# Optimization experiments

Hardware: AMD Instinct MI355X
Metric: run time of the kernel (lower is better)

Reference implementation:

```python
import jax, jax.numpy as jnp
import numpy as np

H = 8          # n_heads
D = 1024       # dim_tgt == dim_mem
DQ = D // H    # per-head dim = 128
BN = 512       # LFFN bottleneck (hardcoded in module)
HID = 1024     # LFFN hidden (hardcoded in module)
B = 16
S_T = 1024     # target length
S_M = 2048     # memory length
SCALE = DQ ** 0.25  # module uses dim_q ** (1/4)
EPS = 1e-5


def _ln(x, g, b):
    m = jnp.mean(x, axis=-1, keepdims=True)
    v = jnp.mean(jnp.square(x - m), axis=-1, keepdims=True)
    return (x - m) * jax.lax.rsqrt(v + EPS) * g + b


def _mhla(xq, xk, xv, Wq, Wk, Wv, Wo, masked):
    # per-head projections: x [b,s,D] x W [H,D,DQ] -> [b,H,s,DQ]
    Q = jnp.einsum('bsq,hqd->bhsd', xq, Wq)
    K = jnp.einsum('bsq,hqd->bhsd', xk, Wk)
    V = jnp.einsum('bsq,hqd->bhsd', xv, Wv)
    if masked:
        s, d = Q.shape[-2], Q.shape[-1]
        # module adds log(triu(ones).T) directly to Q: 0 where d_idx<=t, -inf otherwise
        m = jnp.where(jnp.arange(d)[None, :] <= jnp.arange(s)[:, None], 0.0, -jnp.inf)
        Q = Q + m.astype(Q.dtype)
    # softmax_col(K^T/d_k) over head-dim axis == softmax(K/d_k, axis=-1)
    A = jnp.einsum('bhsd,bhse->bhde', jax.nn.softmax(K / SCALE, axis=-1), V)  # [b,H,DQ,DQ]
    Bm = jnp.einsum('bhsd,bhde->bhse', jax.nn.softmax(Q / SCALE, axis=-1), A)  # [b,H,s,DQ]
    b, h, w, dd = Bm.shape
    # torch .view(b, w, h*d) on contiguous [b,h,w,d]: raw row-major reshape (no transpose)
    Bm = Bm.reshape(b, w, h * dd)
    return Bm @ Wo.T


def setup_inputs():
    key = jax.random.key(0)
    ks = jax.random.split(key, 24)
    r = lambda k, sh, s=0.02: (jax.random.normal(k, sh, jnp.float32) * s)
    return {
        'mem': jax.random.normal(ks[0], (B, S_M, D), jnp.float32),
        'y': jax.random.normal(ks[1], (B, S_T, D), jnp.float32),
        # self-attention (masked)
        'Wq1': r(ks[2], (H, D, DQ)), 'Wk1': r(ks[3], (H, D, DQ)), 'Wv1': r(ks[4], (H, D, DQ)),
        'Wo1': r(ks[5], (D, D)),
        # cross-attention with memory
        'Wq2': r(ks[6], (H, D, DQ)), 'Wk2': r(ks[7], (H, D, DQ)), 'Wv2': r(ks[8], (H, D, DQ)),
        'Wo2': r(ks[9], (D, D)),
        # LFFN (torch Linear weights are [out, in])
        'E1': r(ks[10], (BN, D)), 'D1': r(ks[11], (HID, BN)),
        'E2': r(ks[12], (BN, HID)), 'D2': r(ks[13], (D, BN)),
        # LayerNorm affine params
        'g1': jnp.ones((D,), jnp.float32), 'b1': jnp.zeros((D,), jnp.float32),
        'g2': jnp.ones((D,), jnp.float32), 'b2': jnp.zeros((D,), jnp.float32),
        'g3': jnp.ones((D,), jnp.float32), 'b3': jnp.zeros((D,), jnp.float32),
    }


def reference(mem, y, Wq1, Wk1, Wv1, Wo1, Wq2, Wk2, Wv2, Wo2,
              E1, D1, E2, D2, g1, b1, g2, b2, g3, b3):
    # dropout layers are identity in eval mode
    y = y + _mhla(y, y, y, Wq1, Wk1, Wv1, Wo1, masked=True)
    y = _ln(y, g1, b1)
    y = y + _mhla(y, mem, mem, Wq2, Wk2, Wv2, Wo2, masked=False)
    y = _ln(y, g2, b2)
    # LFFN: E1 -> D1 -> swish -> E2 -> D2
    h = (y @ E1.T) @ D1.T
    h = h * jax.nn.sigmoid(h)
    ffn = (h @ E2.T) @ D2.T
    y = _ln(y + ffn, g3, b3)
    return y
```

## Files before the change

### kernel.cpp

```cpp
#include <hip/hip_runtime.h>
#include <hip/hip_bf16.h>

#define DEVI __device__ __forceinline__

typedef __bf16 bfrag __attribute__((ext_vector_type(8)));
typedef unsigned short us8 __attribute__((ext_vector_type(8)));
typedef float f32x4 __attribute__((ext_vector_type(4)));
typedef unsigned short ushort_t;

static constexpr int NB  = 16;
static constexpr int NH  = 8;
static constexpr int DIM = 1024;
static constexpr int DQh = 128;
static constexpr int ST  = 1024;
static constexpr int SM  = 2048;
static constexpr float INV_SCALE = 0.29730177875068026f;
static constexpr float LN_EPS = 1e-5f;

DEVI ushort_t f2bf(float f) {
  __hip_bfloat16 h = __float2bfloat16(f);
  return __builtin_bit_cast(ushort_t, h);
}
DEVI float bf2f(ushort_t u) {
  return __bfloat162float(__builtin_bit_cast(__hip_bfloat16, u));
}
DEVI bfrag ldfrag(const ushort_t* p) {
  return __builtin_bit_cast(bfrag, *(const us8*)p);
}
DEVI void gl16(const ushort_t* g, ushort_t* l) {
  __builtin_amdgcn_global_load_lds(
      (const __attribute__((address_space(1))) void*)g,
      (__attribute__((address_space(3))) void*)l, 16, 0, 0);
}

enum { ST_BF16 = 0, ST_SWISH = 1, ST_F32RES = 2, ST_SCR = 3, ST_QKV = 4 };

template<int STORE>
__global__ __launch_bounds__(256, 2)
void gemm_bb(const ushort_t* __restrict__ A, const ushort_t* __restrict__ Bt,
             const float* __restrict__ Res,
             ushort_t* __restrict__ Q0, ushort_t* __restrict__ Q1,
             ushort_t* __restrict__ Q2, float* __restrict__ Cf,
             int M, int N, int K, long aZ, long bZ, int logS)
{
  __shared__ ushort_t As[128][32];
  __shared__ ushort_t Bs[128][32];
  const int tid = threadIdx.x;
  int bx = blockIdx.x, by = blockIdx.y;
  if (gridDim.z == 1) {
    const int gx = gridDim.x;
    const int nwg = gx * gridDim.y;
    int bid = by * gx + bx;
    if ((nwg & 7) == 0) bid = (bid & 7) * (nwg >> 3) + (bid >> 3);
    bx = bid % gx; by = bid / gx;
  }
  const int z = blockIdx.z;
  const int m0 = by * 128, n0 = bx * 128;
  A  += aZ * (long)z;
  Bt += bZ * (long)z;

  const int lane = tid & 63;
  const int w = tid >> 6;
  const int wr = (w >> 1) * 64, wc = (w & 1) * 64;
  const int frow = lane & 15;

  const int grow = lane >> 2;
  const int gk = ((lane & 3) ^ ((lane >> 3) & 3)) * 8;
  const ushort_t* Ag = A + (long)(m0 + w * 32 + grow) * K + gk;
  const ushort_t* Bg = Bt + (long)(n0 + w * 32 + grow) * K + gk;

  f32x4 acc[4][4];
  #pragma unroll
  for (int i = 0; i < 4; ++i)
    #pragma unroll
    for (int j = 0; j < 4; ++j) acc[i][j] = f32x4{0.f, 0.f, 0.f, 0.f};

  const int kqs = ((frow >> 1) & 3);
  for (int k0 = 0; k0 < K; k0 += 32) {
    __syncthreads();
    gl16(Ag + k0,               &As[w * 32][0]);
    gl16(Ag + k0 + (long)16 * K, &As[w * 32 + 16][0]);
    gl16(Bg + k0,               &Bs[w * 32][0]);
    gl16(Bg + k0 + (long)16 * K, &Bs[w * 32 + 16][0]);
    __syncthreads();
    const int kq = (lane >> 4) ^ kqs;
    bfrag af[4], bf[4];
    #pragma unroll
    for (int i = 0; i < 4; ++i) af[i] = ldfrag(&As[wr + i * 16 + frow][kq * 8]);
    #pragma unroll
    for (int j = 0; j < 4; ++j) bf[j] = ldfrag(&Bs[wc + j * 16 + frow][kq * 8]);
    #pragma unroll
    for (int i = 0; i < 4; ++i)
      #pragma unroll
      for (int j = 0; j < 4; ++j)
        acc[i][j] = __builtin_amdgcn_mfma_f32_16x16x32_bf16(af[i], bf[j], acc[i][j], 0, 0, 0);
  }

  const int rb = (lane >> 4) * 4;
  if constexpr (STORE == ST_QKV) {
    const int sel = n0 >> 10;
    const int h = (n0 >> 7) & 7;
    ushort_t* __restrict__ Bq = (sel == 0) ? Q0 : ((sel == 1) ? Q1 : Q2);
    const int S = 1 << logS;
    #pragma unroll
    for (int i = 0; i < 4; ++i)
      #pragma unroll
      for (int j = 0; j < 4; ++j)
        #pragma unroll
        for (int e = 0; e < 4; ++e) {
          const int gm = m0 + wr + i * 16 + rb + e;
          const int dq = wc + j * 16 + frow;
          const int b = gm >> logS, s = gm & (S - 1);
          Bq[((long)(h * 16 + b) * S + (long)s) * 128 + dq] = f2bf(acc[i][j][e]);
        }
  } else {
    #pragma unroll
    for (int i = 0; i < 4; ++i)
      #pragma unroll
      for (int j = 0; j < 4; ++j)
        #pragma unroll
        for (int e = 0; e < 4; ++e) {
          const int gm = m0 + wr + i * 16 + rb + e;
          const int gn = n0 + wc + j * 16 + frow;
          float val = acc[i][j][e];
          if constexpr (STORE == ST_SWISH) val = val / (1.0f + __expf(-val));
          if constexpr (STORE == ST_BF16 || STORE == ST_SWISH) {
            Q0[(long)gm * N + gn] = f2bf(val);
          } else if constexpr (STORE == ST_F32RES) {
            Cf[(long)gm * N + gn] = val + Res[(long)gm * N + gn];
          } else if constexpr (STORE == ST_SCR) {
            const int b = z & 15, hh = z >> 4;
            Q0[(long)b * (ST * DIM) + (long)(hh * 128 + (gm >> 3)) * DIM +
               (gm & 7) * 128 + gn] = f2bf(val);
          }
        }
  }
}

__global__ __launch_bounds__(256, 2)
void gemm_ktv(const ushort_t* __restrict__ Kp, const ushort_t* __restrict__ Vp,
              ushort_t* __restrict__ AT, int S)
{
  __shared__ ushort_t As[128][40];
  __shared__ ushort_t Bs[128][40];
  const int tid = threadIdx.x;
  const int z = blockIdx.x;
  const ushort_t* Vb = Vp + (long)z * S * DQh;
  const ushort_t* Kb = Kp + (long)z * S * DQh;
  const int lane = tid & 63;
  const int wr = ((tid >> 6) >> 1) * 64, wc = ((tid >> 6) & 1) * 64;
  const int frow = lane & 15, fk = (lane >> 4) * 8;
  const int c = tid & 127;
  const int sr0 = tid >> 7;

  f32x4 acc[4][4];
  #pragma unroll
  for (int i = 0; i < 4; ++i)
    #pragma unroll
    for (int j = 0; j < 4; ++j) acc[i][j] = f32x4{0.f, 0.f, 0.f, 0.f};

  for (int s0 = 0; s0 < S; s0 += 32) {
    __syncthreads();
    #pragma unroll
    for (int p = 0; p < 16; ++p) {
      const int sr = sr0 + p * 2;
      As[c][sr] = Vb[(long)(s0 + sr) * DQh + c];
      Bs[c][sr] = Kb[(long)(s0 + sr) * DQh + c];
    }
    __syncthreads();
    bfrag af[4], bfv[4];
    #pragma unroll
    for (int i = 0; i < 4; ++i) af[i]  = ldfrag(&As[wr + i * 16 + frow][fk]);
    #pragma unroll
    for (int j = 0; j < 4; ++j) bfv[j] = ldfrag(&Bs[wc + j * 16 + frow][fk]);
    #pragma unroll
    for (int i = 0; i < 4; ++i)
      #pragma unroll
      for (int j = 0; j < 4; ++j)
        acc[i][j] = __builtin_amdgcn_mfma_f32_16x16x32_bf16(af[i], bfv[j], acc[i][j], 0, 0, 0);
  }
  const int rb = (lane >> 4) * 4;
  #pragma unroll
  for (int i = 0; i < 4; ++i)
    #pragma unroll
    for (int j = 0; j < 4; ++j)
      #pragma unroll
      for (int e = 0; e < 4; ++e)
        AT[(long)z * 16384 + (long)(wr + i * 16 + rb + e) * 128 + (wc + j * 16 + frow)] =
            f2bf(acc[i][j][e]);
}

template<bool MASKED>
__global__ __launch_bounds__(256)
void softmax128(ushort_t* __restrict__ X, int smask)
{
  const int row = blockIdx.x * 4 + (threadIdx.x >> 6);
  const int lane = threadIdx.x & 63;
  ushort_t* xr = X + (long)row * 128;
  float x0 = bf2f(xr[lane]) * INV_SCALE;
  float x1 = bf2f(xr[lane + 64]) * INV_SCALE;
  if constexpr (MASKED) {
    const int s = row & smask;
    if (lane > s)      x0 = -3.0e38f;
    if (lane + 64 > s) x1 = -3.0e38f;
  }
  float mx = fmaxf(x0, x1);
  #pragma unroll
  for (int o = 32; o; o >>= 1) mx = fmaxf(mx, __shfl_xor(mx, o));
  const float e0 = __expf(x0 - mx);
  const float e1 = __expf(x1 - mx);
  float sm = e0 + e1;
  #pragma unroll
  for (int o = 32; o; o >>= 1) sm += __shfl_xor(sm, o);
  const float inv = 1.0f / sm;
  xr[lane]      = f2bf(e0 * inv);
  xr[lane + 64] = f2bf(e1 * inv);
}

__global__ __launch_bounds__(256)
void layernorm_k(const float* __restrict__ X, const float* __restrict__ G,
                 const float* __restrict__ Bta, float* __restrict__ Y,
                 ushort_t* __restrict__ Yb)
{
  const int row = blockIdx.x;
  const int t = threadIdx.x;
  const float4 v = *(const float4*)(X + (long)row * DIM + t * 4);
  float s  = v.x + v.y + v.z + v.w;
  float sq = v.x * v.x + v.y * v.y + v.z * v.z + v.w * v.w;
  #pragma unroll
  for (int o = 32; o; o >>= 1) { s += __shfl_xor(s, o); sq += __shfl_xor(sq, o); }
  __shared__ float ps[4], pq[4];
  if ((t & 63) == 0) { ps[t >> 6] = s; pq[t >> 6] = sq; }
  __syncthreads();
  s  = ps[0] + ps[1] + ps[2] + ps[3];
  sq = pq[0] + pq[1] + pq[2] + pq[3];
  const float mean = s * (1.0f / DIM);
  const float var  = sq * (1.0f / DIM) - mean * mean;
  const float rstd = rsqrtf(var + LN_EPS);
  const float4 gv = *(const float4*)(G + t * 4);
  const float4 bv = *(const float4*)(Bta + t * 4);
  float4 o;
  o.x = (v.x - mean) * rstd * gv.x + bv.x;
  o.y = (v.y - mean) * rstd * gv.y + bv.y;
  o.z = (v.z - mean) * rstd * gv.z + bv.z;
  o.w = (v.w - mean) * rstd * gv.w + bv.w;
  *(float4*)(Y + (long)row * DIM + t * 4) = o;
  if (Yb) {
    ushort4 ob = make_ushort4(f2bf(o.x), f2bf(o.y), f2bf(o.z), f2bf(o.w));
    *(ushort4*)(Yb + (long)row * DIM + t * 4) = ob;
  }
}

__global__ __launch_bounds__(256)
void transpose_cast(const float* __restrict__ W, ushort_t* __restrict__ Wt)
{
  __shared__ float tile[32][33];
  const int z = blockIdx.z;
  const int kb = blockIdx.y * 32;
  const int nb = blockIdx.x * 32;
  const float* src = W + (long)z * DIM * DQh;
  ushort_t* dst = Wt + (long)z * DIM * DQh;
  const int tx = threadIdx.x & 31;
  const int ty = threadIdx.x >> 5;
  #pragma unroll
  for (int r = 0; r < 32; r += 8)
    tile[ty + r][tx] = src[(long)(kb + ty + r) * DQh + nb + tx];
  __syncthreads();
  #pragma unroll
  for (int r = 0; r < 32; r += 8)
    dst[(long)(nb + ty + r) * DIM + kb + tx] = f2bf(tile[tx][ty + r]);
}

__global__ __launch_bounds__(256)
void cast_bf16(const float* __restrict__ X, ushort_t* __restrict__ Yq)
{
  const long i = ((long)blockIdx.x * 256 + threadIdx.x) * 4;
  const float4 v = *(const float4*)(X + i);
  ushort4 sv = make_ushort4(f2bf(v.x), f2bf(v.y), f2bf(v.z), f2bf(v.w));
  *(ushort4*)(Yq + i) = sv;
}


extern "C" void kernel_launch(void* const* d_in, const int* in_sizes, int n_in,
                              void* d_out, int out_size, void* d_ws, size_t ws_size,
                              hipStream_t stream)
{
  (void)in_sizes; (void)n_in; (void)out_size; (void)ws_size;
  const float* mem = (const float*)d_in[0];
  const float* y0  = (const float*)d_in[1];
  const float* Wq1 = (const float*)d_in[2];
  const float* Wk1 = (const float*)d_in[3];
  const float* Wv1 = (const float*)d_in[4];
  const float* Wo1 = (const float*)d_in[5];
  const float* Wq2 = (const float*)d_in[6];
  const float* Wk2 = (const float*)d_in[7];
  const float* Wv2 = (const float*)d_in[8];
  const float* Wo2 = (const float*)d_in[9];
  const float* E1  = (const float*)d_in[10];
  const float* D1  = (const float*)d_in[11];
  const float* E2  = (const float*)d_in[12];
  const float* D2  = (const float*)d_in[13];
  const float* g1  = (const float*)d_in[14];
  const float* b1  = (const float*)d_in[15];
  const float* g2  = (const float*)d_in[16];
  const float* b2  = (const float*)d_in[17];
  const float* g3  = (const float*)d_in[18];
  const float* b3  = (const float*)d_in[19];

  char* ws = (char*)d_ws;
  const size_t MB = 1ull << 20;
  ushort_t* wcat1 = (ushort_t*)(ws + 0 * MB);
  ushort_t* wkv2  = (ushort_t*)(ws + 6 * MB);
  ushort_t* wq2t  = (ushort_t*)(ws + 10 * MB);
  ushort_t* wo1b  = (ushort_t*)(ws + 12 * MB);
  ushort_t* wo2b  = (ushort_t*)(ws + 14 * MB);
  ushort_t* e1b   = (ushort_t*)(ws + 16 * MB);
  ushort_t* d1b   = (ushort_t*)(ws + 17 * MB);
  ushort_t* e2b   = (ushort_t*)(ws + 18 * MB);
  ushort_t* d2b   = (ushort_t*)(ws + 19 * MB);
  ushort_t* y0b   = (ushort_t*)(ws + 20 * MB);
  ushort_t* memb  = (ushort_t*)(ws + 52 * MB);
  ushort_t* qbuf  = (ushort_t*)(ws + 116 * MB);
  ushort_t* kbuf  = (ushort_t*)(ws + 148 * MB);
  ushort_t* vbuf  = (ushort_t*)(ws + 212 * MB);
  ushort_t* amatT = (ushort_t*)(ws + 276 * MB);
  ushort_t* attnb = (ushort_t*)(ws + 280 * MB);
  float*    ybuf  = (float*)(ws + 312 * MB);
  ushort_t* ybf   = (ushort_t*)(ws + 376 * MB);
  ushort_t* hbuf  = (ushort_t*)(ws + 408 * MB);
  ushort_t* bn1   = attnb;
  ushort_t* bn2   = qbuf;

  cast_bf16<<<16384, 256, 0, stream>>>(y0, y0b);
  cast_bf16<<<32768, 256, 0, stream>>>(mem, memb);
  transpose_cast<<<dim3(4, 32, 8), 256, 0, stream>>>(Wq1, wcat1);
  transpose_cast<<<dim3(4, 32, 8), 256, 0, stream>>>(Wk1, wcat1 + (1 << 20));
  transpose_cast<<<dim3(4, 32, 8), 256, 0, stream>>>(Wv1, wcat1 + (2 << 20));
  transpose_cast<<<dim3(4, 32, 8), 256, 0, stream>>>(Wk2, wkv2);
  transpose_cast<<<dim3(4, 32, 8), 256, 0, stream>>>(Wv2, wkv2 + (1 << 20));
  transpose_cast<<<dim3(4, 32, 8), 256, 0, stream>>>(Wq2, wq2t);
  cast_bf16<<<1024, 256, 0, stream>>>(Wo1, wo1b);
  cast_bf16<<<1024, 256, 0, stream>>>(Wo2, wo2b);
  cast_bf16<<<512, 256, 0, stream>>>(E1, e1b);
  cast_bf16<<<512, 256, 0, stream>>>(D1, d1b);
  cast_bf16<<<512, 256, 0, stream>>>(E2, e2b);
  cast_bf16<<<512, 256, 0, stream>>>(D2, d2b);

  gemm_bb<ST_QKV><<<dim3(24, 128, 1), 256, 0, stream>>>(
      y0b, wcat1, nullptr, qbuf, kbuf, vbuf, nullptr,
      NB * ST, 3072, DIM, 0, 0, 10);
  softmax128<true><<<NH * NB * ST / 4, 256, 0, stream>>>(qbuf, ST - 1);
  softmax128<false><<<NH * NB * ST / 4, 256, 0, stream>>>(kbuf, 0);
  gemm_ktv<<<NH * NB, 256, 0, stream>>>(kbuf, vbuf, amatT, ST);
  gemm_bb<ST_SCR><<<dim3(1, 8, 128), 256, 0, stream>>>(
      qbuf, amatT, nullptr, attnb, nullptr, nullptr, nullptr,
      ST, DQh, DQh, (long)ST * DQh, 16384, 0);
  gemm_bb<ST_F32RES><<<dim3(8, 128, 1), 256, 0, stream>>>(
      attnb, wo1b, y0, nullptr, nullptr, nullptr, ybuf,
      NB * ST, DIM, DIM, 0, 0, 0);
  layernorm_k<<<NB * ST, 256, 0, stream>>>(ybuf, g1, b1, ybuf, ybf);

  gemm_bb<ST_QKV><<<dim3(8, 128, 1), 256, 0, stream>>>(
      ybf, wq2t, nullptr, qbuf, nullptr, nullptr, nullptr,
      NB * ST, 1024, DIM, 0, 0, 10);
  gemm_bb<ST_QKV><<<dim3(16, 256, 1), 256, 0, stream>>>(
      memb, wkv2, nullptr, kbuf, vbuf, nullptr, nullptr,
      NB * SM, 2048, DIM, 0, 0, 11);
  softmax128<false><<<NH * NB * ST / 4, 256, 0, stream>>>(qbuf, 0);
  softmax128<false><<<NH * NB * SM / 4, 256, 0, stream>>>(kbuf, 0);
  gemm_ktv<<<NH * NB, 256, 0, stream>>>(kbuf, vbuf, amatT, SM);
  gemm_bb<ST_SCR><<<dim3(1, 8, 128), 256, 0, stream>>>(
      qbuf, amatT, nullptr, attnb, nullptr, nullptr, nullptr,
      ST, DQh, DQh, (long)ST * DQh, 16384, 0);
  gemm_bb<ST_F32RES><<<dim3(8, 128, 1), 256, 0, stream>>>(
      attnb, wo2b, ybuf, nullptr, nullptr, nullptr, ybuf,
      NB * ST, DIM, DIM, 0, 0, 0);
  layernorm_k<<<NB * ST, 256, 0, stream>>>(ybuf, g2, b2, ybuf, ybf);

  gemm_bb<ST_BF16><<<dim3(4, 128, 1), 256, 0, stream>>>(
      ybf, e1b, nullptr, bn1, nullptr, nullptr, nullptr,
      NB * ST, 512, DIM, 0, 0, 0);
  gemm_bb<ST_SWISH><<<dim3(8, 128, 1), 256, 0, stream>>>(
      bn1, d1b, nullptr, hbuf, nullptr, nullptr, nullptr,
      NB * ST, DIM, 512, 0, 0, 0);
  gemm_bb<ST_BF16><<<dim3(4, 128, 1), 256, 0, stream>>>(
      hbuf, e2b, nullptr, bn2, nullptr, nullptr, nullptr,
      NB * ST, 512, DIM, 0, 0, 0);
  gemm_bb<ST_F32RES><<<dim3(8, 128, 1), 256, 0, stream>>>(
      bn2, d2b, ybuf, nullptr, nullptr, nullptr, ybuf,
      NB * ST, DIM, 512, 0, 0, 0);
  layernorm_k<<<NB * ST, 256, 0, stream>>>(ybuf, g3, b3, (float*)d_out, nullptr);
}
```

Baseline: 1.007 ms.

## Fuse head softmax into QKV GEMM epilogue, split K^T V, use bf16 residual stream

The per-row softmax over the head dimension for Q and K now runs inside the QKV projection GEMM epilogue. Row max and sum are combined across the two column warps through shared memory, which removes the separate softmax kernels and their extra read and write of Q and K. The K^T·V reduction is split along sequence chunks into fp32 partials plus a small reduce kernel, giving more blocks to fill the GPU. The residual and LayerNorm path now keeps activations in bf16 instead of fp32 to cut memory traffic, at the cost of lower precision in the residual sums.

```diff
diff --git a/kernel.cpp b/kernel.cpp
--- a/kernel.cpp
+++ b/kernel.cpp
@@ -33,18 +33,20 @@
       (__attribute__((address_space(3))) void*)l, 16, 0, 0);
 }
 
-enum { ST_BF16 = 0, ST_SWISH = 1, ST_F32RES = 2, ST_SCR = 3, ST_QKV = 4 };
+enum { ST_BF16 = 0, ST_SWISH = 1, ST_RESB = 2, ST_SCR = 3, ST_QKV = 4 };
 
 template<int STORE>
 __global__ __launch_bounds__(256, 2)
 void gemm_bb(const ushort_t* __restrict__ A, const ushort_t* __restrict__ Bt,
-             const float* __restrict__ Res,
-             ushort_t* __restrict__ Q0, ushort_t* __restrict__ Q1,
-             ushort_t* __restrict__ Q2, float* __restrict__ Cf,
-             int M, int N, int K, long aZ, long bZ, int logS)
+             const ushort_t* __restrict__ ResB,
+             ushort_t* __restrict__ P0, ushort_t* __restrict__ P1,
+             ushort_t* __restrict__ P2,
+             int M, int N, int K, long aZ, long bZ,
+             int logS, int smflags, int maskflags)
 {
   __shared__ ushort_t As[128][32];
   __shared__ ushort_t Bs[128][32];
+  __shared__ float msx[4][64][2];
   const int tid = threadIdx.x;
   int bx = blockIdx.x, by = blockIdx.y;
   if (gridDim.z == 1) {
@@ -63,6 +65,7 @@
   const int w = tid >> 6;
   const int wr = (w >> 1) * 64, wc = (w & 1) * 64;
   const int frow = lane & 15;
+  const int q = lane >> 4;
 
   const int grow = lane >> 2;
   const int gk = ((lane & 3) ^ ((lane >> 3) & 3)) * 8;
@@ -78,12 +81,12 @@
   const int kqs = ((frow >> 1) & 3);
   for (int k0 = 0; k0 < K; k0 += 32) {
     __syncthreads();
-    gl16(Ag + k0,               &As[w * 32][0]);
+    gl16(Ag + k0,                &As[w * 32][0]);
     gl16(Ag + k0 + (long)16 * K, &As[w * 32 + 16][0]);
-    gl16(Bg + k0,               &Bs[w * 32][0]);
+    gl16(Bg + k0,                &Bs[w * 32][0]);
     gl16(Bg + k0 + (long)16 * K, &Bs[w * 32 + 16][0]);
     __syncthreads();
-    const int kq = (lane >> 4) ^ kqs;
+    const int kq = (q ^ kqs);
     bfrag af[4], bf[4];
     #pragma unroll
     for (int i = 0; i < 4; ++i) af[i] = ldfrag(&As[wr + i * 16 + frow][kq * 8]);
@@ -96,11 +99,89 @@
         acc[i][j] = __builtin_amdgcn_mfma_f32_16x16x32_bf16(af[i], bf[j], acc[i][j], 0, 0, 0);
   }
 
-  const int rb = (lane >> 4) * 4;
+  const int rb = q * 4;
   if constexpr (STORE == ST_QKV) {
     const int sel = n0 >> 10;
+    const bool dosm   = (smflags >> sel) & 1;
+    const bool domask = (maskflags >> sel) & 1;
+    const int smask = (1 << logS) - 1;
+    if (dosm) {
+      #pragma unroll
+      for (int i = 0; i < 4; ++i)
+        #pragma unroll
+        for (int e = 0; e < 4; ++e) {
+          const int slim = (m0 + wr + i * 16 + rb + e) & smask;
+          #pragma unroll
+          for (int j = 0; j < 4; ++j) {
+            const int dq = wc + j * 16 + frow;
+            float v = acc[i][j][e] * INV_SCALE;
+            if (domask && dq > slim) v = -3.0e38f;
+            acc[i][j][e] = v;
+          }
+        }
+      float m_ie[4][4], s_ie[4][4];
+      #pragma unroll
+      for (int i = 0; i < 4; ++i)
+        #pragma unroll
+        for (int e = 0; e < 4; ++e) {
+          float m = fmaxf(fmaxf(acc[i][0][e], acc[i][1][e]),
+                          fmaxf(acc[i][2][e], acc[i][3][e]));
+          m = fmaxf(m, __shfl_xor(m, 1));
+          m = fmaxf(m, __shfl_xor(m, 2));
+          m = fmaxf(m, __shfl_xor(m, 4));
+          m = fmaxf(m, __shfl_xor(m, 8));
+          m_ie[i][e] = m;
+        }
+      #pragma unroll
+      for (int i = 0; i < 4; ++i)
+        #pragma unroll
+        for (int j = 0; j < 4; ++j)
+          #pragma unroll
+          for (int e = 0; e < 4; ++e)
+            acc[i][j][e] = __expf(acc[i][j][e] - m_ie[i][e]);
+      #pragma unroll
+      for (int i = 0; i < 4; ++i)
+        #pragma unroll
+        for (int e = 0; e < 4; ++e) {
+          float s = acc[i][0][e] + acc[i][1][e] + acc[i][2][e] + acc[i][3][e];
+          s += __shfl_xor(s, 1);
+          s += __shfl_xor(s, 2);
+          s += __shfl_xor(s, 4);
+          s += __shfl_xor(s, 8);
+          s_ie[i][e] = s;
+        }
+      if (frow == 0) {
+        #pragma unroll
+        for (int i = 0; i < 4; ++i)
+          #pragma unroll
+          for (int e = 0; e < 4; ++e) {
+            msx[w][i * 16 + rb + e][0] = m_ie[i][e];
+            msx[w][i * 16 + rb + e][1] = s_ie[i][e];
+          }
+      }
+      __syncthreads();
+      #pragma unroll
+      for (int i = 0; i < 4; ++i)
+        #pragma unroll
+        for (int e = 0; e < 4; ++e) {
+          const int idx = i * 16 + rb + e;
+          const float mo = msx[w ^ 1][idx][0];
+          const float so = msx[w ^ 1][idx][1];
+          const float mj = fmaxf(m_ie[i][e], mo);
+          const float sj = s_ie[i][e] * __expf(m_ie[i][e] - mj) +
+                           so * __expf(mo - mj);
+          m_ie[i][e] = __expf(m_ie[i][e] - mj) / sj;
+        }
+      #pragma unroll
+      for (int i = 0; i < 4; ++i)
+        #pragma unroll
+        for (int j = 0; j < 4; ++j)
+          #pragma unroll
+          for (int e = 0; e < 4; ++e)
+            acc[i][j][e] *= m_ie[i][e];
+    }
     const int h = (n0 >> 7) & 7;
-    ushort_t* __restrict__ Bq = (sel == 0) ? Q0 : ((sel == 1) ? Q1 : Q2);
+    ushort_t* __restrict__ Bq = (sel == 0) ? P0 : ((sel == 1) ? P1 : P2);
     const int S = 1 << logS;
     #pragma unroll
     for (int i = 0; i < 4; ++i)
@@ -115,38 +196,41 @@
         }
   } else {
     #pragma unroll
-    for (int i = 0; i < 4; ++i)
-      #pragma unroll
-      for (int j = 0; j < 4; ++j)
+    for (int i = 0; i < 4; ++i) {
+      #pragma unroll
+      for (int j = 0; j < 4; ++j) {
         #pragma unroll
         for (int e = 0; e < 4; ++e) {
           const int gm = m0 + wr + i * 16 + rb + e;
           const int gn = n0 + wc + j * 16 + frow;
           float val = acc[i][j][e];
           if constexpr (STORE == ST_SWISH) val = val / (1.0f + __expf(-val));
-          if constexpr (STORE == ST_BF16 || STORE == ST_SWISH) {
-            Q0[(long)gm * N + gn] = f2bf(val);
-          } else if constexpr (STORE == ST_F32RES) {
-            Cf[(long)gm * N + gn] = val + Res[(long)gm * N + gn];
-          } else if constexpr (STORE == ST_SCR) {
+          if constexpr (STORE == ST_RESB)  val += bf2f(ResB[(long)gm * N + gn]);
+          if constexpr (STORE == ST_SCR) {
             const int b = z & 15, hh = z >> 4;
-            Q0[(long)b * (ST * DIM) + (long)(hh * 128 + (gm >> 3)) * DIM +
+            P0[(long)b * (ST * DIM) + (long)(hh * 128 + (gm >> 3)) * DIM +
                (gm & 7) * 128 + gn] = f2bf(val);
+          } else {
+            P0[(long)gm * N + gn] = f2bf(val);
           }
         }
+      }
+    }
   }
 }
 
 __global__ __launch_bounds__(256, 2)
 void gemm_ktv(const ushort_t* __restrict__ Kp, const ushort_t* __restrict__ Vp,
-              ushort_t* __restrict__ AT, int S)
+              float* __restrict__ P, int S, int SC)
 {
   __shared__ ushort_t As[128][40];
   __shared__ ushort_t Bs[128][40];
   const int tid = threadIdx.x;
   const int z = blockIdx.x;
-  const ushort_t* Vb = Vp + (long)z * S * DQh;
-  const ushort_t* Kb = Kp + (long)z * S * DQh;
+  const int ch = blockIdx.y;
+  const long base = ((long)z * S + (long)ch * SC) * DQh;
+  const ushort_t* Vb = Vp + base;
+  const ushort_t* Kb = Kp + base;
   const int lane = tid & 63;
   const int wr = ((tid >> 6) >> 1) * 64, wc = ((tid >> 6) & 1) * 64;
   const int frow = lane & 15, fk = (lane >> 4) * 8;
@@ -159,7 +243,7 @@
     #pragma unroll
     for (int j = 0; j < 4; ++j) acc[i][j] = f32x4{0.f, 0.f, 0.f, 0.f};
 
-  for (int s0 = 0; s0 < S; s0 += 32) {
+  for (int s0 = 0; s0 < SC; s0 += 32) {
     __syncthreads();
     #pragma unroll
     for (int p = 0; p < 16; ++p) {
@@ -179,6 +263,7 @@
       for (int j = 0; j < 4; ++j)
         acc[i][j] = __builtin_amdgcn_mfma_f32_16x16x32_bf16(af[i], bfv[j], acc[i][j], 0, 0, 0);
   }
+  float* Pz = P + ((long)ch * 128 + z) * 16384;
   const int rb = (lane >> 4) * 4;
   #pragma unroll
   for (int i = 0; i < 4; ++i)
@@ -186,47 +271,33 @@
     for (int j = 0; j < 4; ++j)
       #pragma unroll
       for (int e = 0; e < 4; ++e)
-        AT[(long)z * 16384 + (long)(wr + i * 16 + rb + e) * 128 + (wc + j * 16 + frow)] =
-            f2bf(acc[i][j][e]);
-}
-
-template<bool MASKED>
+        Pz[(long)(wr + i * 16 + rb + e) * 128 + (wc + j * 16 + frow)] = acc[i][j][e];
+}
+
 __global__ __launch_bounds__(256)
-void softmax128(ushort_t* __restrict__ X, int smask)
-{
-  const int row = blockIdx.x * 4 + (threadIdx.x >> 6);
-  const int lane = threadIdx.x & 63;
-  ushort_t* xr = X + (long)row * 128;
-  float x0 = bf2f(xr[lane]) * INV_SCALE;
-  float x1 = bf2f(xr[lane + 64]) * INV_SCALE;
-  if constexpr (MASKED) {
-    const int s = row & smask;
-    if (lane > s)      x0 = -3.0e38f;
-    if (lane + 64 > s) x1 = -3.0e38f;
-  }
-  float mx = fmaxf(x0, x1);
-  #pragma unroll
-  for (int o = 32; o; o >>= 1) mx = fmaxf(mx, __shfl_xor(mx, o));
-  const float e0 = __expf(x0 - mx);
-  const float e1 = __expf(x1 - mx);
-  float sm = e0 + e1;
-  #pragma unroll
-  for (int o = 32; o; o >>= 1) sm += __shfl_xor(sm, o);
-  const float inv = 1.0f / sm;
-  xr[lane]      = f2bf(e0 * inv);
-  xr[lane + 64] = f2bf(e1 * inv);
+void ktv_reduce(const float* __restrict__ P, ushort_t* __restrict__ AT, int nch)
+{
+  const long i = ((long)blockIdx.x * 256 + threadIdx.x) * 4;
+  float4 s = *(const float4*)(P + i);
+  for (int c = 1; c < nch; ++c) {
+    const float4 v = *(const float4*)(P + (long)c * 2097152 + i);
+    s.x += v.x; s.y += v.y; s.z += v.z; s.w += v.w;
+  }
+  ushort4 o = make_ushort4(f2bf(s.x), f2bf(s.y), f2bf(s.z), f2bf(s.w));
+  *(ushort4*)(AT + i) = o;
 }
 
 __global__ __launch_bounds__(256)
-void layernorm_k(const float* __restrict__ X, const float* __restrict__ G,
-                 const float* __restrict__ Bta, float* __restrict__ Y,
-                 ushort_t* __restrict__ Yb)
+void layernorm_b(const ushort_t* __restrict__ X, const float* __restrict__ G,
+                 const float* __restrict__ Bta, ushort_t* __restrict__ Yb,
+                 float* __restrict__ Yf)
 {
   const int row = blockIdx.x;
   const int t = threadIdx.x;
-  const float4 v = *(const float4*)(X + (long)row * DIM + t * 4);
-  float s  = v.x + v.y + v.z + v.w;
-  float sq = v.x * v.x + v.y * v.y + v.z * v.z + v.w * v.w;
+  const ushort4 xu = *(const ushort4*)(X + (long)row * DIM + t * 4);
+  float x0 = bf2f(xu.x), x1 = bf2f(xu.y), x2 = bf2f(xu.z), x3 = bf2f(xu.w);
+  float s  = x0 + x1 + x2 + x3;
+  float sq = x0 * x0 + x1 * x1 + x2 * x2 + x3 * x3;
   #pragma unroll
   for (int o = 32; o; o >>= 1) { s += __shfl_xor(s, o); sq += __shfl_xor(sq, o); }
   __shared__ float ps[4], pq[4];
@@ -239,15 +310,17 @@
   const float rstd = rsqrtf(var + LN_EPS);
   const float4 gv = *(const float4*)(G + t * 4);
   const float4 bv = *(const float4*)(Bta + t * 4);
-  float4 o;
-  o.x = (v.x - mean) * rstd * gv.x + bv.x;
-  o.y = (v.y - mean) * rstd * gv.y + bv.y;
-  o.z = (v.z - mean) * rstd * gv.z + bv.z;
-  o.w = (v.w - mean) * rstd * gv.w + bv.w;
-  *(float4*)(Y + (long)row * DIM + t * 4) = o;
+  float o0 = (x0 - mean) * rstd * gv.x + bv.x;
+  float o1 = (x1 - mean) * rstd * gv.y + bv.y;
+  float o2 = (x2 - mean) * rstd * gv.z + bv.z;
+  float o3 = (x3 - mean) * rstd * gv.w + bv.w;
   if (Yb) {
-    ushort4 ob = make_ushort4(f2bf(o.x), f2bf(o.y), f2bf(o.z), f2bf(o.w));
+    ushort4 ob = make_ushort4(f2bf(o0), f2bf(o1), f2bf(o2), f2bf(o3));
     *(ushort4*)(Yb + (long)row * DIM + t * 4) = ob;
+  }
+  if (Yf) {
+    float4 of; of.x = o0; of.y = o1; of.z = o2; of.w = o3;
+    *(float4*)(Yf + (long)row * DIM + t * 4) = of;
   }
 }
 
@@ -325,9 +398,11 @@
   ushort_t* vbuf  = (ushort_t*)(ws + 212 * MB);
   ushort_t* amatT = (ushort_t*)(ws + 276 * MB);
   ushort_t* attnb = (ushort_t*)(ws + 280 * MB);
-  float*    ybuf  = (float*)(ws + 312 * MB);
-  ushort_t* ybf   = (ushort_t*)(ws + 376 * MB);
+  ushort_t* ybr   = (ushort_t*)(ws + 312 * MB);
+  ushort_t* ybnA  = (ushort_t*)(ws + 344 * MB);
+  ushort_t* ybnB  = (ushort_t*)(ws + 376 * MB);
   ushort_t* hbuf  = (ushort_t*)(ws + 408 * MB);
+  float*    pbuf  = (float*)(ws + 440 * MB);
   ushort_t* bn1   = attnb;
   ushort_t* bn2   = qbuf;
 
@@ -347,47 +422,39 @@
   cast_bf16<<<512, 256, 0, stream>>>(D2, d2b);
 
   gemm_bb<ST_QKV><<<dim3(24, 128, 1), 256, 0, stream>>>(
-      y0b, wcat1, nullptr, qbuf, kbuf, vbuf, nullptr,
-      NB * ST, 3072, DIM, 0, 0, 10);
-  softmax128<true><<<NH * NB * ST / 4, 256, 0, stream>>>(qbuf, ST - 1);
-  softmax128<false><<<NH * NB * ST / 4, 256, 0, stream>>>(kbuf, 0);
-  gemm_ktv<<<NH * NB, 256, 0, stream>>>(kbuf, vbuf, amatT, ST);
+      y0b, wcat1, nullptr, qbuf, kbuf, vbuf, NB * ST, 3072, DIM, 0, 0,
+      10,  0b011,  0b001);
+  gemm_ktv<<<dim3(128, 2), 256, 0, stream>>>(kbuf, vbuf, pbuf, ST, 512);
+  ktv_reduce<<<2048, 256, 0, stream>>>(pbuf, amatT, 2);
   gemm_bb<ST_SCR><<<dim3(1, 8, 128), 256, 0, stream>>>(
-      qbuf, amatT, nullptr, attnb, nullptr, nullptr, nullptr,
-      ST, DQh, DQh, (long)ST * DQh, 16384, 0);
-  gemm_bb<ST_F32RES><<<dim3(8, 128, 1), 256, 0, stream>>>(
-      attnb, wo1b, y0, nullptr, nullptr, nullptr, ybuf,
-      NB * ST, DIM, DIM, 0, 0, 0);
-  layernorm_k<<<NB * ST, 256, 0, stream>>>(ybuf, g1, b1, ybuf, ybf);
+      qbuf, amatT, nullptr, attnb, nullptr, nullptr,
+      ST, DQh, DQh, (long)ST * DQh, 16384, 0, 0, 0);
+  gemm_bb<ST_RESB><<<dim3(8, 128, 1), 256, 0, stream>>>(
+      attnb, wo1b, y0b, ybr, nullptr, nullptr, NB * ST, DIM, DIM, 0, 0, 0, 0, 0);
+  layernorm_b<<<NB * ST, 256, 0, stream>>>(ybr, g1, b1, ybnA, nullptr);
 
   gemm_bb<ST_QKV><<<dim3(8, 128, 1), 256, 0, stream>>>(
-      ybf, wq2t, nullptr, qbuf, nullptr, nullptr, nullptr,
-      NB * ST, 1024, DIM, 0, 0, 10);
+      ybnA, wq2t, nullptr, qbuf, nullptr, nullptr, NB * ST, 1024, DIM, 0, 0,
+      10, 0b001, 0);
   gemm_bb<ST_QKV><<<dim3(16, 256, 1), 256, 0, stream>>>(
-      memb, wkv2, nullptr, kbuf, vbuf, nullptr, nullptr,
-      NB * SM, 2048, DIM, 0, 0, 11);
-  softmax128<false><<<NH * NB * ST / 4, 256, 0, stream>>>(qbuf, 0);
-  softmax128<false><<<NH * NB * SM / 4, 256, 0, stream>>>(kbuf, 0);
-  gemm_ktv<<<NH * NB, 256, 0, stream>>>(kbuf, vbuf, amatT, SM);
+      memb, wkv2, nullptr, kbuf, vbuf, nullptr, NB * SM, 2048, DIM, 0, 0,
+      11, 0b001, 0);
+  gemm_ktv<<<dim3(128, 4), 256, 0, stream>>>(kbuf, vbuf, pbuf, SM, 512);
+  ktv_reduce<<<2048, 256, 0, stream>>>(pbuf, amatT, 4);
   gemm_bb<ST_SCR><<<dim3(1, 8, 128), 256, 0, stream>>>(
-      qbuf, amatT, nullptr, attnb, nullptr, nullptr, nullptr,
-      ST, DQh, DQh, (long)ST * DQh, 16384, 0);
-  gemm_bb<ST_F32RES><<<dim3(8, 128, 1), 256, 0, stream>>>(
-      attnb, wo2b, ybuf, nullptr, nullptr, nullptr, ybuf,
-      NB * ST, DIM, DIM, 0, 0, 0);
-  layernorm_k<<<NB * ST, 256, 0, stream>>>(ybuf, g2, b2, ybuf, ybf);
+      qbuf, amatT, nullptr, attnb, nullptr, nullptr,
+      ST, DQh, DQh, (long)ST * DQh, 16384, 0, 0, 0);
+  gemm_bb<ST_RESB><<<dim3(8, 128, 1), 256, 0, stream>>>(
+      attnb, wo2b, ybnA, ybr, nullptr, nullptr, NB * ST, DIM, DIM, 0, 0, 0, 0, 0);
+  layernorm_b<<<NB * ST, 256, 0, stream>>>(ybr, g2, b2, ybnB, nullptr);
 
   gemm_bb<ST_BF16><<<dim3(4, 128, 1), 256, 0, stream>>>(
-      ybf, e1b, nullptr, bn1, nullptr, nullptr, nullptr,
-      NB * ST, 512, DIM, 0, 0, 0);
+      ybnB, e1b, nullptr, bn1, nullptr, nullptr, NB * ST, 512, DIM, 0, 0, 0, 0, 0);
   gemm_bb<ST_SWISH><<<dim3(8, 128, 1), 256, 0, stream>>>(
-      bn1, d1b, nullptr, hbuf, nullptr, nullptr, nullptr,
-      NB * ST, DIM, 512, 0, 0, 0);
+      bn1, d1b, nullptr, hbuf, nullptr, nullptr, NB * ST, DIM, 512, 0, 0, 0, 0, 0);
   gemm_bb<ST_BF16><<<dim3(4, 128, 1), 256, 0, stream>>>(
-      hbuf, e2b, nullptr, bn2, nullptr, nullptr, nullptr,
-      NB * ST, 512, DIM, 0, 0, 0);
-  gemm_bb<ST_F32RES><<<dim3(8, 128, 1), 256, 0, stream>>>(
-      bn2, d2b, ybuf, nullptr, nullptr, nullptr, ybuf,
-      NB * ST, DIM, 512, 0, 0, 0);
-  layernorm_k<<<NB * ST, 256, 0, stream>>>(ybuf, g3, b3, (float*)d_out, nullptr);
-}
+      hbuf, e2b, nullptr, bn2, nullptr, nullptr, NB * ST, 512, DIM, 0, 0, 0, 0, 0);
+  gemm_bb<ST_RESB><<<dim3(8, 128, 1), 256, 0, stream>>>(
+      bn2, d2b, ybnB, ybr, nullptr, nullptr, NB * ST, DIM, 512, 0, 0, 0, 0, 0);
+  layernorm_b<<<NB * ST, 256, 0, stream>>>(ybr, g3, b3, nullptr, (float*)d_out);
+}
```

After: 958.8 us. 4.8% less time.
